# Performance work log

Measured on AMD Instinct MI355X. Metric: run time of the kernel, lower is better.

The kernel has to match this reference:

```python
import jax, jax.numpy as jnp
import numpy as np

N_SRC = 50000
N_DST = 50000
E = 400000
D_IN = 256
D_OUT = 256


def setup_inputs() -> dict:
    key = jax.random.key(0)
    k1, k2, k3, k4, k5 = jax.random.split(key, 5)
    src_feats = jax.random.normal(k1, (N_SRC, D_IN), dtype=jnp.float32)
    edge_feats = jax.random.normal(k2, (E, D_IN), dtype=jnp.float32)
    src_idx = jax.random.randint(k3, (E,), 0, N_SRC, dtype=jnp.int32)
    dst_idx = jax.random.randint(k4, (E,), 0, N_DST, dtype=jnp.int32)
    # xavier_uniform over [2*in_feat, out_feat] (transposed init in torch, same bound)
    fan_in, fan_out = 2 * D_IN, D_OUT
    bound = np.sqrt(6.0 / (fan_in + fan_out))
    weights = jax.random.uniform(k5, (2 * D_IN, D_OUT), dtype=jnp.float32,
                                 minval=-bound, maxval=bound)
    h_bias = jnp.zeros((D_OUT,), dtype=jnp.float32)
    return {"src_feats": src_feats, "edge_feats": edge_feats,
            "src_idx": src_idx, "dst_idx": dst_idx,
            "weights": weights, "h_bias": h_bias, "num_dst": N_DST}


def reference(src_feats, edge_feats, src_idx, dst_idx, weights, h_bias, num_dst):
    # edge_feat_mp_op == 'concat':
    #   m = concat([src_h, e_h], -1) @ W  ==  src_h @ W[:D] + e_h @ W[D:]
    d = src_feats.shape[1]
    m = src_feats[src_idx] @ weights[:d] + edge_feats @ weights[d:]  # [E, D_OUT]
    # in-degree normalization: norm = in_deg(dst)^{-0.5}, applied per edge (e_mul_v)
    deg = jax.ops.segment_sum(jnp.ones((m.shape[0],), jnp.float32), dst_idx,
                              num_segments=num_dst)
    norm = jnp.where(deg > 0, jax.lax.rsqrt(jnp.maximum(deg, 1.0)), 0.0)
    h = jax.ops.segment_sum(m * norm[dst_idx][:, None], dst_idx,
                            num_segments=num_dst)  # [N_DST, D_OUT]
    return h + h_bias
```

## Files before the change

### kernel.cpp

```cpp
#include <hip/hip_runtime.h>

typedef __attribute__((ext_vector_type(8))) short bf16x8;
typedef __attribute__((ext_vector_type(4))) float f32x4;

#define D_IN 256
#define D_OUT 256
#define KDIM 512
#define GM 32
#define G_ROWS 8
#define CAP 32

static __device__ __forceinline__ unsigned short f2bf(float f) {
    union { float f; unsigned int u; } x; x.f = f;
    unsigned int r = (x.u + 0x7FFFu + ((x.u >> 16) & 1u)) >> 16;
    return (unsigned short)r;
}

#define GLOAD16(gp, lp) __builtin_amdgcn_global_load_lds(                    \
    (const __attribute__((address_space(1))) void*)(gp),                     \
    (__attribute__((address_space(3))) void*)(lp), 16, 0, 0)
#define GLOAD16NT(gp, lp) __builtin_amdgcn_global_load_lds(                  \
    (const __attribute__((address_space(1))) void*)(gp),                     \
    (__attribute__((address_space(3))) void*)(lp), 16, 0, 2)

__global__ void zero_wfrag_kernel(int* __restrict__ cursor, int n, int zblocks,
                                  const float* __restrict__ W, unsigned short* __restrict__ wf) {
    int b = blockIdx.x;
    if (b < zblocks) {
        int i = b * 256 + threadIdx.x;
        if (i < n) cursor[i] = 0;
    } else {
        int t = (b - zblocks) * 256 + threadIdx.x;
        if (t < 16 * 16 * 64) {
            int l  = t & 63;
            int kk = (t >> 6) & 15;
            int nt = t >> 10;
            int c  = nt * 16 + (l & 15);
            int kb = kk * 32 + (l >> 4) * 8;
            union { unsigned short u[8]; uint4 v; } pk;
#pragma unroll
            for (int j = 0; j < 8; ++j) pk.u[j] = f2bf(W[(size_t)(kb + j) * D_OUT + c]);
            *reinterpret_cast<uint4*>(&wf[(size_t)t * 8]) = pk.v;
        }
    }
}

__global__ void scatter_kernel(const int* __restrict__ dst, const int* __restrict__ src_idx,
                               int* __restrict__ cursor, int2* __restrict__ rec, int E) {
    int e2 = (blockIdx.x * 256 + threadIdx.x) * 2;
    if (e2 + 1 < E) {
        int2 d = *reinterpret_cast<const int2*>(&dst[e2]);
        int2 s = *reinterpret_cast<const int2*>(&src_idx[e2]);
        int p0 = atomicAdd(&cursor[d.x], 1);
        if (p0 < CAP) rec[(size_t)d.x * CAP + p0] = make_int2(e2, s.x);
        int p1 = atomicAdd(&cursor[d.y], 1);
        if (p1 < CAP) rec[(size_t)d.y * CAP + p1] = make_int2(e2 + 1, s.y);
    } else if (e2 < E) {
        int d = dst[e2];
        int p = atomicAdd(&cursor[d], 1);
        if (p < CAP) rec[(size_t)d * CAP + p] = make_int2(e2, src_idx[e2]);
    }
}

__global__ __launch_bounds__(256) void agg_kernel(
    const float* __restrict__ src_feats,
    const float* __restrict__ edge_feats,
    const int2* __restrict__ rec,
    const int* __restrict__ cursor,
    unsigned short* __restrict__ agg,
    int n_dst)
{
    __shared__ __align__(16) float fb[4][2][2][KDIM];
    __shared__ __align__(16) int2 idb[4][G_ROWS * CAP];

    const int wv = threadIdx.x >> 6;
    const int ln = threadIdx.x & 63;
    const int rowbase = (blockIdx.x * 4 + wv) * G_ROWS;

    int cnt = 0;
    if (ln < G_ROWS) {
        int i = rowbase + ln;
        if (i < n_dst) { cnt = cursor[i]; if (cnt > CAP) cnt = CAP; }
    }
    int incl = cnt;
#pragma unroll
    for (int o = 1; o < 64; o <<= 1) { int u = __shfl_up(incl, o); if (ln >= o) incl += u; }
    const int excl = incl - cnt;
    const int nE = __shfl(incl, G_ROWS - 1);

    {
        const char* gsrc = (const char*)(rec + (size_t)rowbase * CAP);
        GLOAD16(gsrc + ln * 16, (char*)&idb[wv][0]);
        GLOAD16(gsrc + 1024 + ln * 16, (char*)&idb[wv][0] + 1024);
    }
    asm volatile("s_waitcnt vmcnt(0)" ::: "memory");
    __builtin_amdgcn_sched_barrier(0);

    float4 a0 = make_float4(0.f, 0.f, 0.f, 0.f);
    float4 a1 = make_float4(0.f, 0.f, 0.f, 0.f);
    int consRow = 0;
    int consEnd = __shfl(incl, 0);
    int issRow = 0;
    int issEnd = consEnd;

    auto flush = [&]() {
        int gr = rowbase + consRow;
        if (gr < n_dst) {
            ushort4 p0, p1;
            p0.x = f2bf(a0.x); p0.y = f2bf(a0.y); p0.z = f2bf(a0.z); p0.w = f2bf(a0.w);
            p1.x = f2bf(a1.x); p1.y = f2bf(a1.y); p1.z = f2bf(a1.z); p1.w = f2bf(a1.w);
            *reinterpret_cast<ushort4*>(&agg[(size_t)gr * KDIM + ln * 4]) = p0;
            *reinterpret_cast<ushort4*>(&agg[(size_t)gr * KDIM + D_IN + ln * 4]) = p1;
        }
        a0 = make_float4(0.f, 0.f, 0.f, 0.f);
        a1 = make_float4(0.f, 0.f, 0.f, 0.f);
    };

    auto issue = [&](int ci) {
        int buf = ci & 1;
#pragma unroll
        for (int t = 0; t < 2; ++t) {
            int ja = ci * 2 + t;
            int sid = 0, eid = 0;
            if (ja < nE) {
                while (ja >= issEnd) { ++issRow; issEnd = __shfl(incl, issRow); }
                int st = __shfl(excl, issRow);
                int2 v = idb[wv][issRow * CAP + (ja - st)];
                eid = v.x; sid = v.y;
            }
            float* lp = &fb[wv][buf][t][0];
            GLOAD16(src_feats  + (size_t)sid * D_IN + ln * 4, lp);
            GLOAD16NT(edge_feats + (size_t)eid * D_IN + ln * 4, lp + D_IN);
        }
    };

    const int nCh = (nE + 1) >> 1;
    issue(0); issue(1);
    for (int ci = 0; ci < nCh; ++ci) {
        asm volatile("s_waitcnt vmcnt(4)" ::: "memory");
        __builtin_amdgcn_sched_barrier(0);
        int buf = ci & 1;
#pragma unroll
        for (int t = 0; t < 2; ++t) {
            int ja = ci * 2 + t;
            if (ja >= nE) break;
            while (ja >= consEnd) {
                flush();
                ++consRow;
                consEnd = __shfl(incl, consRow);
            }
            float4 v0 = *reinterpret_cast<const float4*>(&fb[wv][buf][t][ln * 4]);
            float4 v1 = *reinterpret_cast<const float4*>(&fb[wv][buf][t][D_IN + ln * 4]);
            a0.x += v0.x; a0.y += v0.y; a0.z += v0.z; a0.w += v0.w;
            a1.x += v1.x; a1.y += v1.y; a1.z += v1.z; a1.w += v1.w;
        }
        issue(ci + 2);
    }
    asm volatile("s_waitcnt vmcnt(0)" ::: "memory");
    __builtin_amdgcn_sched_barrier(0);
    while (consRow < G_ROWS) { flush(); ++consRow; }
}

__global__ __launch_bounds__(256) void gemm_kernel(
    const unsigned short* __restrict__ agg,
    const unsigned short* __restrict__ wfrag,
    const int* __restrict__ cursor,
    const float* __restrict__ bias,
    float* __restrict__ out,
    int n_dst)
{
    __shared__ __align__(16) unsigned short As[2 * GM * 256];

    const int wv = threadIdx.x >> 6;
    const int ln = threadIdx.x & 63;
    const int lrow = ln & 15;
    const int lgrp = ln >> 4;
    const int base = blockIdx.x * GM;

#pragma unroll
    for (int h = 0; h < 2; ++h) {
#pragma unroll
        for (int q = 0; q < 4; ++q) {
            int p = q * 4 + wv;
            int r = 2 * p + (ln >> 5);
            int gr = base + r; if (gr >= n_dst) gr = n_dst - 1;
            int sg = (ln & 31) ^ (r & 7);
            GLOAD16(agg + (size_t)gr * KDIM + h * 256 + sg * 8,
                    (char*)As + h * 16384 + p * 1024);
        }
    }

    f32x4 acc[2][4];
#pragma unroll
    for (int m = 0; m < 2; ++m)
#pragma unroll
        for (int n = 0; n < 4; ++n) acc[m][n] = (f32x4)(0.0f);

    asm volatile("s_waitcnt vmcnt(4)" ::: "memory");
    __builtin_amdgcn_s_barrier();
    __builtin_amdgcn_sched_barrier(0);

#pragma unroll
    for (int kk = 0; kk < 8; ++kk) {
        bf16x8 A[2];
#pragma unroll
        for (int m = 0; m < 2; ++m) {
            int r = m * 16 + lrow;
            int g = (kk * 4 + lgrp) ^ (r & 7);
            A[m] = *reinterpret_cast<const bf16x8*>((const char*)As + r * 512 + g * 16);
        }
#pragma unroll
        for (int n = 0; n < 4; ++n) {
            int nt = wv * 4 + n;
            bf16x8 B = *reinterpret_cast<const bf16x8*>(&wfrag[(((size_t)nt * 16 + kk) * 64 + ln) * 8]);
#pragma unroll
            for (int m = 0; m < 2; ++m)
                acc[m][n] = __builtin_amdgcn_mfma_f32_16x16x32_bf16(A[m], B, acc[m][n], 0, 0, 0);
        }
    }

    asm volatile("s_waitcnt vmcnt(0)" ::: "memory");
    __builtin_amdgcn_s_barrier();
    __builtin_amdgcn_sched_barrier(0);

#pragma unroll
    for (int kk = 8; kk < 16; ++kk) {
        bf16x8 A[2];
#pragma unroll
        for (int m = 0; m < 2; ++m) {
            int r = m * 16 + lrow;
            int g = ((kk - 8) * 4 + lgrp) ^ (r & 7);
            A[m] = *reinterpret_cast<const bf16x8*>((const char*)As + 16384 + r * 512 + g * 16);
        }
#pragma unroll
        for (int n = 0; n < 4; ++n) {
            int nt = wv * 4 + n;
            bf16x8 B = *reinterpret_cast<const bf16x8*>(&wfrag[(((size_t)nt * 16 + kk) * 64 + ln) * 8]);
#pragma unroll
            for (int m = 0; m < 2; ++m)
                acc[m][n] = __builtin_amdgcn_mfma_f32_16x16x32_bf16(A[m], B, acc[m][n], 0, 0, 0);
        }
    }

    float bias_r[4];
#pragma unroll
    for (int n = 0; n < 4; ++n) bias_r[n] = bias[wv * 64 + n * 16 + lrow];

#pragma unroll
    for (int m = 0; m < 2; ++m) {
#pragma unroll
        for (int j = 0; j < 4; ++j) {
            int r = base + m * 16 + lgrp * 4 + j;
            if (r < n_dst) {
                int dg = cursor[r];
                float nv = (dg > 0) ? rsqrtf((float)dg) : 0.0f;
#pragma unroll
                for (int n = 0; n < 4; ++n)
                    out[(size_t)r * D_OUT + wv * 64 + n * 16 + lrow] = acc[m][n][j] * nv + bias_r[n];
            }
        }
    }
}

extern "C" void kernel_launch(void* const* d_in, const int* in_sizes, int n_in,
                              void* d_out, int out_size, void* d_ws, size_t ws_size,
                              hipStream_t stream) {
    const float* src_feats  = (const float*)d_in[0];
    const float* edge_feats = (const float*)d_in[1];
    const int*   src_idx    = (const int*)d_in[2];
    const int*   dst_idx    = (const int*)d_in[3];
    const float* weights    = (const float*)d_in[4];
    const float* h_bias     = (const float*)d_in[5];

    const int E     = in_sizes[2];
    const int n_dst = out_size / D_OUT;
    float* out = (float*)d_out;

    char* ws = (char*)d_ws;
    size_t agg_bytes = (size_t)n_dst * KDIM * 2;
    unsigned short* agg   = (unsigned short*)ws;
    unsigned short* wfrag = (unsigned short*)(ws + agg_bytes);
    int2* rec     = (int2*)(ws + agg_bytes + 262144);
    size_t rec_bytes = (size_t)n_dst * CAP * 8 + 4096;
    int*  cursor  = (int*)(ws + agg_bytes + 262144 + rec_bytes);

    const int ZB = (n_dst + 255) / 256;
    const int SB = (E / 2 + 255) / 256;
    const int NB = (n_dst + 4 * G_ROWS - 1) / (4 * G_ROWS);

    zero_wfrag_kernel<<<ZB + 64, 256, 0, stream>>>(cursor, n_dst, ZB, weights, wfrag);
    scatter_kernel<<<SB, 256, 0, stream>>>(dst_idx, src_idx, cursor, rec, E);

    agg_kernel<<<NB, 256, 0, stream>>>(
        src_feats, edge_feats, rec, cursor, agg, n_dst);
    gemm_kernel<<<NB, 256, 0, stream>>>(
        agg, wfrag, cursor, h_bias, out, n_dst);
}
```

Before: 209.0 us.

## Precompute src_feats @ W_src per source node and gather projected bf16 rows

Splits the concat GEMM so each source node is projected through the top half of W once, stored as bf16, and folded into the scatter kernel launch. The aggregation then gathers 512-byte bf16 projected rows instead of 1 KB fp32 source rows, and the final GEMM only multiplies the aggregated edge features by the bottom half of W, adding the summed projections in the epilogue. This cuts gather bandwidth and GEMM K-depth, at the cost of an extra full-source GEMM pass and an extra bf16 rounding of the projected values.

```diff
diff --git a/kernel.cpp b/kernel.cpp
--- a/kernel.cpp
+++ b/kernel.cpp
@@ -5,8 +5,6 @@
 
 #define D_IN 256
 #define D_OUT 256
-#define KDIM 512
-#define GM 32
 #define G_ROWS 8
 #define CAP 32
 
@@ -14,6 +12,9 @@
     union { float f; unsigned int u; } x; x.f = f;
     unsigned int r = (x.u + 0x7FFFu + ((x.u >> 16) & 1u)) >> 16;
     return (unsigned short)r;
+}
+static __device__ __forceinline__ float bf2f(unsigned short u) {
+    union { unsigned int i; float f; } x; x.i = ((unsigned int)u) << 16; return x.f;
 }
 
 #define GLOAD16(gp, lp) __builtin_amdgcn_global_load_lds(                    \
@@ -24,53 +25,128 @@
     (__attribute__((address_space(3))) void*)(lp), 16, 0, 2)
 
 __global__ void zero_wfrag_kernel(int* __restrict__ cursor, int n, int zblocks,
-                                  const float* __restrict__ W, unsigned short* __restrict__ wf) {
+                                  const float* __restrict__ W,
+                                  unsigned short* __restrict__ wfs,
+                                  unsigned short* __restrict__ wfe) {
     int b = blockIdx.x;
     if (b < zblocks) {
         int i = b * 256 + threadIdx.x;
         if (i < n) cursor[i] = 0;
-    } else {
-        int t = (b - zblocks) * 256 + threadIdx.x;
-        if (t < 16 * 16 * 64) {
-            int l  = t & 63;
-            int kk = (t >> 6) & 15;
-            int nt = t >> 10;
-            int c  = nt * 16 + (l & 15);
-            int kb = kk * 32 + (l >> 4) * 8;
-            union { unsigned short u[8]; uint4 v; } pk;
-#pragma unroll
-            for (int j = 0; j < 8; ++j) pk.u[j] = f2bf(W[(size_t)(kb + j) * D_OUT + c]);
-            *reinterpret_cast<uint4*>(&wf[(size_t)t * 8]) = pk.v;
-        }
-    }
-}
-
-__global__ void scatter_kernel(const int* __restrict__ dst, const int* __restrict__ src_idx,
-                               int* __restrict__ cursor, int2* __restrict__ rec, int E) {
-    int e2 = (blockIdx.x * 256 + threadIdx.x) * 2;
-    if (e2 + 1 < E) {
-        int2 d = *reinterpret_cast<const int2*>(&dst[e2]);
-        int2 s = *reinterpret_cast<const int2*>(&src_idx[e2]);
-        int p0 = atomicAdd(&cursor[d.x], 1);
-        if (p0 < CAP) rec[(size_t)d.x * CAP + p0] = make_int2(e2, s.x);
-        int p1 = atomicAdd(&cursor[d.y], 1);
-        if (p1 < CAP) rec[(size_t)d.y * CAP + p1] = make_int2(e2 + 1, s.y);
-    } else if (e2 < E) {
-        int d = dst[e2];
-        int p = atomicAdd(&cursor[d], 1);
-        if (p < CAP) rec[(size_t)d * CAP + p] = make_int2(e2, src_idx[e2]);
+        return;
+    }
+    int s = (b - zblocks) >> 5;
+    int t = ((b - zblocks) & 31) * 256 + threadIdx.x;
+    int l  = t & 63;
+    int kk = (t >> 6) & 7;
+    int nt = t >> 9;
+    int c  = nt * 16 + (l & 15);
+    int kb = s * 256 + kk * 32 + (l >> 4) * 8;
+    union { unsigned short u[8]; uint4 v; } pk;
+#pragma unroll
+    for (int j = 0; j < 8; ++j) pk.u[j] = f2bf(W[(size_t)(kb + j) * D_OUT + c]);
+    unsigned short* wf = s ? wfe : wfs;
+    *reinterpret_cast<uint4*>(&wf[(size_t)t * 8]) = pk.v;
+}
+
+__global__ __launch_bounds__(256) void combo_kernel(
+    const int* __restrict__ dst, const int* __restrict__ src_idx,
+    int* __restrict__ cursor, int2* __restrict__ rec, int E, int SB,
+    const float* __restrict__ src_feats, const unsigned short* __restrict__ wfs,
+    unsigned short* __restrict__ Xs, int n_src)
+{
+    __shared__ __align__(16) float As[32 * 256];
+
+    if (blockIdx.x < SB) {
+        int e2 = (blockIdx.x * 256 + threadIdx.x) * 2;
+        if (e2 + 1 < E) {
+            int2 d = *reinterpret_cast<const int2*>(&dst[e2]);
+            int2 s = *reinterpret_cast<const int2*>(&src_idx[e2]);
+            int p0 = atomicAdd(&cursor[d.x], 1);
+            if (p0 < CAP) rec[(size_t)d.x * CAP + p0] = make_int2(e2, s.x);
+            int p1 = atomicAdd(&cursor[d.y], 1);
+            if (p1 < CAP) rec[(size_t)d.y * CAP + p1] = make_int2(e2 + 1, s.y);
+        } else if (e2 < E) {
+            int d = dst[e2];
+            int p = atomicAdd(&cursor[d], 1);
+            if (p < CAP) rec[(size_t)d * CAP + p] = make_int2(e2, src_idx[e2]);
+        }
+        return;
+    }
+
+    const int wv = threadIdx.x >> 6;
+    const int ln = threadIdx.x & 63;
+    const int lrow = ln & 15;
+    const int lgrp = ln >> 4;
+    const int base = (blockIdx.x - SB) * 32;
+
+#pragma unroll
+    for (int q = 0; q < 8; ++q) {
+        int r = q * 4 + wv;
+        int gr = base + r; if (gr >= n_src) gr = n_src - 1;
+        GLOAD16(src_feats + (size_t)gr * D_IN + ((ln ^ (r & 7)) * 4),
+                (char*)As + r * 1024);
+    }
+    asm volatile("s_waitcnt vmcnt(0)" ::: "memory");
+    __builtin_amdgcn_s_barrier();
+    __builtin_amdgcn_sched_barrier(0);
+
+    f32x4 acc[2][4];
+#pragma unroll
+    for (int m = 0; m < 2; ++m)
+#pragma unroll
+        for (int n = 0; n < 4; ++n) acc[m][n] = (f32x4)(0.0f);
+
+#pragma unroll
+    for (int kk = 0; kk < 8; ++kk) {
+        bf16x8 A[2];
+#pragma unroll
+        for (int m = 0; m < 2; ++m) {
+            int r = m * 16 + lrow;
+            int pi = kk * 4 + lgrp;
+            int g0 = (2 * pi) ^ (r & 7);
+            int g1 = (2 * pi + 1) ^ (r & 7);
+            float4 f0 = *reinterpret_cast<const float4*>((const char*)As + r * 1024 + g0 * 16);
+            float4 f1 = *reinterpret_cast<const float4*>((const char*)As + r * 1024 + g1 * 16);
+            union { unsigned short u[8]; bf16x8 v; } pk;
+            pk.u[0] = f2bf(f0.x); pk.u[1] = f2bf(f0.y); pk.u[2] = f2bf(f0.z); pk.u[3] = f2bf(f0.w);
+            pk.u[4] = f2bf(f1.x); pk.u[5] = f2bf(f1.y); pk.u[6] = f2bf(f1.z); pk.u[7] = f2bf(f1.w);
+            A[m] = pk.v;
+        }
+#pragma unroll
+        for (int n = 0; n < 4; ++n) {
+            int nt = wv * 4 + n;
+            bf16x8 B = *reinterpret_cast<const bf16x8*>(&wfs[(((size_t)nt * 8 + kk) * 64 + ln) * 8]);
+#pragma unroll
+            for (int m = 0; m < 2; ++m)
+                acc[m][n] = __builtin_amdgcn_mfma_f32_16x16x32_bf16(A[m], B, acc[m][n], 0, 0, 0);
+        }
+    }
+
+#pragma unroll
+    for (int m = 0; m < 2; ++m) {
+#pragma unroll
+        for (int j = 0; j < 4; ++j) {
+            int r = base + m * 16 + lgrp * 4 + j;
+            if (r < n_src) {
+#pragma unroll
+                for (int n = 0; n < 4; ++n)
+                    Xs[(size_t)r * D_OUT + wv * 64 + n * 16 + lrow] = f2bf(acc[m][n][j]);
+            }
+        }
     }
 }
 
 __global__ __launch_bounds__(256) void agg_kernel(
-    const float* __restrict__ src_feats,
+    const unsigned short* __restrict__ Xs,
     const float* __restrict__ edge_feats,
     const int2* __restrict__ rec,
     const int* __restrict__ cursor,
-    unsigned short* __restrict__ agg,
+    unsigned short* __restrict__ Ae,
+    unsigned short* __restrict__ Sx,
     int n_dst)
 {
-    __shared__ __align__(16) float fb[4][2][2][KDIM];
+    __shared__ __align__(16) float fbe[4][2][2][D_IN];
+    __shared__ __align__(16) unsigned short sxb[4][2][512];
     __shared__ __align__(16) int2 idb[4][G_ROWS * CAP];
 
     const int wv = threadIdx.x >> 6;
@@ -96,8 +172,8 @@
     asm volatile("s_waitcnt vmcnt(0)" ::: "memory");
     __builtin_amdgcn_sched_barrier(0);
 
-    float4 a0 = make_float4(0.f, 0.f, 0.f, 0.f);
-    float4 a1 = make_float4(0.f, 0.f, 0.f, 0.f);
+    float4 ae = make_float4(0.f, 0.f, 0.f, 0.f);
+    float4 ax = make_float4(0.f, 0.f, 0.f, 0.f);
     int consRow = 0;
     int consEnd = __shfl(incl, 0);
     int issRow = 0;
@@ -106,38 +182,39 @@
     auto flush = [&]() {
         int gr = rowbase + consRow;
         if (gr < n_dst) {
-            ushort4 p0, p1;
-            p0.x = f2bf(a0.x); p0.y = f2bf(a0.y); p0.z = f2bf(a0.z); p0.w = f2bf(a0.w);
-            p1.x = f2bf(a1.x); p1.y = f2bf(a1.y); p1.z = f2bf(a1.z); p1.w = f2bf(a1.w);
-            *reinterpret_cast<ushort4*>(&agg[(size_t)gr * KDIM + ln * 4]) = p0;
-            *reinterpret_cast<ushort4*>(&agg[(size_t)gr * KDIM + D_IN + ln * 4]) = p1;
-        }
-        a0 = make_float4(0.f, 0.f, 0.f, 0.f);
-        a1 = make_float4(0.f, 0.f, 0.f, 0.f);
+            ushort4 pe, px;
+            pe.x = f2bf(ae.x); pe.y = f2bf(ae.y); pe.z = f2bf(ae.z); pe.w = f2bf(ae.w);
+            px.x = f2bf(ax.x); px.y = f2bf(ax.y); px.z = f2bf(ax.z); px.w = f2bf(ax.w);
+            *reinterpret_cast<ushort4*>(&Ae[(size_t)gr * D_OUT + ln * 4]) = pe;
+            *reinterpret_cast<ushort4*>(&Sx[(size_t)gr * D_OUT + ln * 4]) = px;
+        }
+        ae = make_float4(0.f, 0.f, 0.f, 0.f);
+        ax = make_float4(0.f, 0.f, 0.f, 0.f);
     };
 
     auto issue = [&](int ci) {
         int buf = ci & 1;
+        int sid[2] = {0, 0}, eid[2] = {0, 0};
 #pragma unroll
         for (int t = 0; t < 2; ++t) {
             int ja = ci * 2 + t;
-            int sid = 0, eid = 0;
             if (ja < nE) {
                 while (ja >= issEnd) { ++issRow; issEnd = __shfl(incl, issRow); }
                 int st = __shfl(excl, issRow);
                 int2 v = idb[wv][issRow * CAP + (ja - st)];
-                eid = v.x; sid = v.y;
+                eid[t] = v.x; sid[t] = v.y;
             }
-            float* lp = &fb[wv][buf][t][0];
-            GLOAD16(src_feats  + (size_t)sid * D_IN + ln * 4, lp);
-            GLOAD16NT(edge_feats + (size_t)eid * D_IN + ln * 4, lp + D_IN);
-        }
+        }
+        GLOAD16NT(edge_feats + (size_t)eid[0] * D_IN + ln * 4, &fbe[wv][buf][0][0]);
+        GLOAD16NT(edge_feats + (size_t)eid[1] * D_IN + ln * 4, &fbe[wv][buf][1][0]);
+        int sidt = (ln < 32) ? sid[0] : sid[1];
+        GLOAD16((const char*)Xs + (size_t)sidt * 512 + (ln & 31) * 16, (char*)&sxb[wv][buf][0]);
     };
 
     const int nCh = (nE + 1) >> 1;
     issue(0); issue(1);
     for (int ci = 0; ci < nCh; ++ci) {
-        asm volatile("s_waitcnt vmcnt(4)" ::: "memory");
+        asm volatile("s_waitcnt vmcnt(3)" ::: "memory");
         __builtin_amdgcn_sched_barrier(0);
         int buf = ci & 1;
 #pragma unroll
@@ -149,10 +226,10 @@
                 ++consRow;
                 consEnd = __shfl(incl, consRow);
             }
-            float4 v0 = *reinterpret_cast<const float4*>(&fb[wv][buf][t][ln * 4]);
-            float4 v1 = *reinterpret_cast<const float4*>(&fb[wv][buf][t][D_IN + ln * 4]);
-            a0.x += v0.x; a0.y += v0.y; a0.z += v0.z; a0.w += v0.w;
-            a1.x += v1.x; a1.y += v1.y; a1.z += v1.z; a1.w += v1.w;
+            float4 ve = *reinterpret_cast<const float4*>(&fbe[wv][buf][t][ln * 4]);
+            ushort4 vs = *reinterpret_cast<const ushort4*>((const char*)&sxb[wv][buf][0] + t * 512 + ln * 8);
+            ae.x += ve.x; ae.y += ve.y; ae.z += ve.z; ae.w += ve.w;
+            ax.x += bf2f(vs.x); ax.y += bf2f(vs.y); ax.z += bf2f(vs.z); ax.w += bf2f(vs.w);
         }
         issue(ci + 2);
     }
@@ -162,80 +239,54 @@
 }
 
 __global__ __launch_bounds__(256) void gemm_kernel(
-    const unsigned short* __restrict__ agg,
-    const unsigned short* __restrict__ wfrag,
+    const unsigned short* __restrict__ Ae,
+    const unsigned short* __restrict__ Sx,
+    const unsigned short* __restrict__ wfe,
     const int* __restrict__ cursor,
     const float* __restrict__ bias,
     float* __restrict__ out,
     int n_dst)
 {
-    __shared__ __align__(16) unsigned short As[2 * GM * 256];
+    __shared__ __align__(16) unsigned short As[32 * 256];
 
     const int wv = threadIdx.x >> 6;
     const int ln = threadIdx.x & 63;
     const int lrow = ln & 15;
     const int lgrp = ln >> 4;
-    const int base = blockIdx.x * GM;
-
-#pragma unroll
-    for (int h = 0; h < 2; ++h) {
-#pragma unroll
-        for (int q = 0; q < 4; ++q) {
-            int p = q * 4 + wv;
-            int r = 2 * p + (ln >> 5);
-            int gr = base + r; if (gr >= n_dst) gr = n_dst - 1;
-            int sg = (ln & 31) ^ (r & 7);
-            GLOAD16(agg + (size_t)gr * KDIM + h * 256 + sg * 8,
-                    (char*)As + h * 16384 + p * 1024);
-        }
-    }
-
-    f32x4 acc[2][4];
-#pragma unroll
-    for (int m = 0; m < 2; ++m)
-#pragma unroll
-        for (int n = 0; n < 4; ++n) acc[m][n] = (f32x4)(0.0f);
-
-    asm volatile("s_waitcnt vmcnt(4)" ::: "memory");
-    __builtin_amdgcn_s_barrier();
-    __builtin_amdgcn_sched_barrier(0);
-
-#pragma unroll
-    for (int kk = 0; kk < 8; ++kk) {
-        bf16x8 A[2];
-#pragma unroll
-        for (int m = 0; m < 2; ++m) {
-            int r = m * 16 + lrow;
-            int g = (kk * 4 + lgrp) ^ (r & 7);
-            A[m] = *reinterpret_cast<const bf16x8*>((const char*)As + r * 512 + g * 16);
-        }
-#pragma unroll
-        for (int n = 0; n < 4; ++n) {
-            int nt = wv * 4 + n;
-            bf16x8 B = *reinterpret_cast<const bf16x8*>(&wfrag[(((size_t)nt * 16 + kk) * 64 + ln) * 8]);
-#pragma unroll
-            for (int m = 0; m < 2; ++m)
-                acc[m][n] = __builtin_amdgcn_mfma_f32_16x16x32_bf16(A[m], B, acc[m][n], 0, 0, 0);
-        }
-    }
-
+    const int base = blockIdx.x * 32;
+
+#pragma unroll
+    for (int q = 0; q < 4; ++q) {
+        int p = q * 4 + wv;
+        int rr = 2 * p + (ln >> 5);
+        int gr = base + rr; if (gr >= n_dst) gr = n_dst - 1;
+        GLOAD16((const char*)Ae + (size_t)gr * 512 + (size_t)(((ln & 31) ^ (rr & 7)) * 16),
+                (char*)As + p * 1024);
+    }
     asm volatile("s_waitcnt vmcnt(0)" ::: "memory");
     __builtin_amdgcn_s_barrier();
     __builtin_amdgcn_sched_barrier(0);
 
-#pragma unroll
-    for (int kk = 8; kk < 16; ++kk) {
+    f32x4 acc[2][4];
+#pragma unroll
+    for (int m = 0; m < 2; ++m)
+#pragma unroll
+        for (int n = 0; n < 4; ++n) acc[m][n] = (f32x4)(0.0f);
+
+#pragma unroll
+    for (int kk = 0; kk < 8; ++kk) {
         bf16x8 A[2];
 #pragma unroll
         for (int m = 0; m < 2; ++m) {
             int r = m * 16 + lrow;
-            int g = ((kk - 8) * 4 + lgrp) ^ (r & 7);
-            A[m] = *reinterpret_cast<const bf16x8*>((const char*)As + 16384 + r * 512 + g * 16);
+            int dg = (kk * 4 + lgrp) ^ (r & 7);
+            A[m] = *reinterpret_cast<const bf16x8*>(
+                (const char*)As + (r >> 1) * 1024 + (r & 1) * 512 + dg * 16);
         }
 #pragma unroll
         for (int n = 0; n < 4; ++n) {
             int nt = wv * 4 + n;
-            bf16x8 B = *reinterpret_cast<const bf16x8*>(&wfrag[(((size_t)nt * 16 + kk) * 64 + ln) * 8]);
+            bf16x8 B = *reinterpret_cast<const bf16x8*>(&wfe[(((size_t)nt * 8 + kk) * 64 + ln) * 8]);
 #pragma unroll
             for (int m = 0; m < 2; ++m)
                 acc[m][n] = __builtin_amdgcn_mfma_f32_16x16x32_bf16(A[m], B, acc[m][n], 0, 0, 0);
@@ -255,8 +306,11 @@
                 int dg = cursor[r];
                 float nv = (dg > 0) ? rsqrtf((float)dg) : 0.0f;
 #pragma unroll
-                for (int n = 0; n < 4; ++n)
-                    out[(size_t)r * D_OUT + wv * 64 + n * 16 + lrow] = acc[m][n][j] * nv + bias_r[n];
+                for (int n = 0; n < 4; ++n) {
+                    int col = wv * 64 + n * 16 + lrow;
+                    float sxv = bf2f(Sx[(size_t)r * D_OUT + col]);
+                    out[(size_t)r * D_OUT + col] = (acc[m][n][j] + sxv) * nv + bias_r[n];
+                }
             }
         }
     }
@@ -273,26 +327,30 @@
     const float* h_bias     = (const float*)d_in[5];
 
     const int E     = in_sizes[2];
+    const int n_src = in_sizes[0] / D_IN;
     const int n_dst = out_size / D_OUT;
     float* out = (float*)d_out;
 
     char* ws = (char*)d_ws;
-    size_t agg_bytes = (size_t)n_dst * KDIM * 2;
-    unsigned short* agg   = (unsigned short*)ws;
-    unsigned short* wfrag = (unsigned short*)(ws + agg_bytes);
-    int2* rec     = (int2*)(ws + agg_bytes + 262144);
+    size_t xs_bytes = (size_t)n_src * D_OUT * 2;
+    size_t ad_bytes = (size_t)n_dst * D_OUT * 2;
+    unsigned short* Xs  = (unsigned short*)ws;
+    unsigned short* Ae  = (unsigned short*)(ws + xs_bytes);
+    unsigned short* Sx  = (unsigned short*)(ws + xs_bytes + ad_bytes);
+    unsigned short* wfs = (unsigned short*)(ws + xs_bytes + 2 * ad_bytes);
+    unsigned short* wfe = wfs + 65536;
+    int2* rec    = (int2*)(ws + xs_bytes + 2 * ad_bytes + 262144);
     size_t rec_bytes = (size_t)n_dst * CAP * 8 + 4096;
-    int*  cursor  = (int*)(ws + agg_bytes + 262144 + rec_bytes);
+    int* cursor  = (int*)(ws + xs_bytes + 2 * ad_bytes + 262144 + rec_bytes);
 
     const int ZB = (n_dst + 255) / 256;
     const int SB = (E / 2 + 255) / 256;
+    const int XB = (n_src + 31) / 32;
     const int NB = (n_dst + 4 * G_ROWS - 1) / (4 * G_ROWS);
 
-    zero_wfrag_kernel<<<ZB + 64, 256, 0, stream>>>(cursor, n_dst, ZB, weights, wfrag);
-    scatter_kernel<<<SB, 256, 0, stream>>>(dst_idx, src_idx, cursor, rec, E);
-
-    agg_kernel<<<NB, 256, 0, stream>>>(
-        src_feats, edge_feats, rec, cursor, agg, n_dst);
-    gemm_kernel<<<NB, 256, 0, stream>>>(
-        agg, wfrag, cursor, h_bias, out, n_dst);
-}
+    zero_wfrag_kernel<<<ZB + 64, 256, 0, stream>>>(cursor, n_dst, ZB, weights, wfs, wfe);
+    combo_kernel<<<SB + XB, 256, 0, stream>>>(dst_idx, src_idx, cursor, rec, E, SB,
+                                              src_feats, wfs, Xs, n_src);
+    agg_kernel<<<NB, 256, 0, stream>>>(Xs, edge_feats, rec, cursor, Ae, Sx, n_dst);
+    gemm_kernel<<<NB, 256, 0, stream>>>(Ae, Sx, wfe, cursor, h_bias, out, n_dst);
+}
```

Result: faster. 194.7 us (median of 2 runs) (-6.8%).
